# Optimization experiments

Hardware: AMD Instinct MI355X
Metric: run time of the kernel (lower is better)

The kernel has to match this reference:

```python
import jax, jax.numpy as jnp
import numpy as np
from jax import lax

D = 256
B, W = 16, 32


def setup_inputs() -> dict:
    key = jax.random.key(0)
    ks = jax.random.split(key, 5)
    x = jax.random.normal(ks[0], (B, D, W, W), dtype=jnp.float32)
    w_qkv = jax.random.normal(ks[1], (3 * D, D), dtype=jnp.float32) * (1.0 / np.sqrt(D))
    b_qkv = jax.random.normal(ks[2], (3 * D,), dtype=jnp.float32) * 0.01
    w_out = jax.random.normal(ks[3], (D, D, 3, 3), dtype=jnp.float32) * (1.0 / np.sqrt(9 * D))
    b_out = jax.random.normal(ks[4], (D,), dtype=jnp.float32) * 0.01
    alpha = jnp.ones((), dtype=jnp.float32)
    return {"x": x, "w_qkv": w_qkv, "b_qkv": b_qkv, "w_out": w_out, "b_out": b_out, "alpha": alpha}


def reference(x, w_qkv, b_qkv, w_out, b_out, alpha):
    Bb, C, H, Ww = x.shape  # C == D, H == Ww
    N = H * Ww
    # 1x1 conv qkv projection
    qkv = jnp.einsum('bchw,oc->bohw', x, w_qkv) + b_qkv[None, :, None, None]
    q, k, v = jnp.split(qkv, 3, axis=1)
    q = q.reshape(Bb, C, N)
    k = k.reshape(Bb, C, N)
    v = v.reshape(Bb, C, N)
    scale = 1.0 / (C ** 0.5)
    attn = jax.nn.softmax(jnp.einsum('bcq,bck->bqk', q, k) * scale, axis=-1)  # [B,N,N]
    # faithful to torch: (B,N,C) memory-reinterpreted to (B,C,H,W)
    out = jnp.einsum('bqk,bck->bqc', attn, v).reshape(Bb, C, H, Ww)
    x = x + alpha * jax.nn.relu(out)
    conv = lax.conv_general_dilated(
        x, w_out, window_strides=(1, 1), padding='SAME',
        dimension_numbers=('NCHW', 'OIHW', 'NCHW')) + b_out[None, :, None, None]
    x = x + alpha * jax.nn.relu(conv)
    return x
```

## Files before the change

kernel.cpp:

```cpp
#include <hip/hip_runtime.h>
#include <cmath>

namespace {

constexpr int Dc  = 256;
constexpr int NB  = 16;
constexpr int NSP = 1024;
constexpr int OC3 = 768;

typedef __attribute__((ext_vector_type(8))) short  short8;
typedef __attribute__((ext_vector_type(8))) ushort ushort8;
typedef __attribute__((ext_vector_type(4))) ushort ushort4_v;
typedef __attribute__((ext_vector_type(4))) float  f32x4;

__device__ inline ushort f2bf(float f) {
  unsigned u = __builtin_bit_cast(unsigned, f);
  unsigned r = (u + 0x7FFFu + ((u >> 16) & 1u)) >> 16;
  return (ushort)r;
}
__device__ inline float bf2f(ushort u) {
  return __builtin_bit_cast(float, (unsigned)u << 16);
}

__device__ __forceinline__ void dma16(const ushort* g, ushort* l) {
  __builtin_amdgcn_global_load_lds(
      (const __attribute__((address_space(1))) unsigned int*)(const void*)g,
      (__attribute__((address_space(3))) unsigned int*)(void*)l, 16, 0, 0);
}

template<int BM>
__device__ __forceinline__ void mfma_core(
    const ushort* __restrict__ Abase, int lda,
    const ushort* __restrict__ Bbase, int ldb,
    int m0, int n0, int K, f32x4 (&acc)[BM / 32][4])
{
  constexpr int MI    = BM / 32;
  constexpr int AI    = BM / 64;
  constexpr int NLOAD = AI + 2;
  constexpr int BUFSZ = BM * 32 + 128 * 32;
  __shared__ ushort LDS[3 * BUFSZ];

  const int t = threadIdx.x;
  const int lane = t & 63, wid = t >> 6;
  const int wm = (wid >> 1) * (BM / 2);
  const int wo = (wid & 1) * 64;
  const int lm = lane & 15, lk = lane >> 4;
  const int aph = lk ^ ((lm >> 1) & 3);

  const int lrow = lane >> 2;
  const int niter = K >> 5;

  auto issue = [&](int kk) {
    const int c0 = kk << 5;
    ushort* buf = &LDS[(kk % 3) * BUFSZ];
#pragma unroll
    for (int i = 0; i < AI; ++i) {
      const int r0 = (i * 4 + wid) * 16;
      const int row = r0 + lrow;
      const int chunk = (lane & 3) ^ ((row >> 1) & 3);
      dma16(Abase + (size_t)(m0 + row) * lda + c0 + chunk * 8, buf + r0 * 32);
    }
#pragma unroll
    for (int i = 0; i < 2; ++i) {
      const int r0 = (i * 4 + wid) * 16;
      const int row = r0 + lrow;
      const int chunk = (lane & 3) ^ ((row >> 1) & 3);
      dma16(Bbase + (size_t)(n0 + row) * ldb + c0 + chunk * 8,
            buf + BM * 32 + r0 * 32);
    }
  };

  issue(0);
  issue(1);

  for (int kk = 0; kk < niter; ++kk) {
    __builtin_amdgcn_sched_barrier(0);
    if (kk < niter - 1) {
      if constexpr (NLOAD == 4)
        asm volatile("s_waitcnt vmcnt(4) lgkmcnt(0)" ::: "memory");
      else
        asm volatile("s_waitcnt vmcnt(3) lgkmcnt(0)" ::: "memory");
    } else {
      asm volatile("s_waitcnt vmcnt(0) lgkmcnt(0)" ::: "memory");
    }
    __builtin_amdgcn_s_barrier();
    __builtin_amdgcn_sched_barrier(0);
    if (kk + 2 < niter) issue(kk + 2);

    const ushort* Ab = &LDS[(kk % 3) * BUFSZ];
    const ushort* Bb = Ab + BM * 32;
    short8 af[MI], bw[4];
#pragma unroll
    for (int mi = 0; mi < MI; ++mi)
      af[mi] = *(const short8*)&Ab[(wm + mi * 16 + lm) * 32 + aph * 8];
#pragma unroll
    for (int oi = 0; oi < 4; ++oi)
      bw[oi] = *(const short8*)&Bb[(wo + oi * 16 + lm) * 32 + aph * 8];
#pragma unroll
    for (int mi = 0; mi < MI; ++mi)
#pragma unroll
      for (int oi = 0; oi < 4; ++oi)
        acc[mi][oi] = __builtin_amdgcn_mfma_f32_16x16x32_bf16(
            af[mi], bw[oi], acc[mi][oi], 0, 0, 0);
  }
}

__global__ __launch_bounds__(256) void k0_prep(
    const float* __restrict__ x, const float* __restrict__ w_qkv,
    const float* __restrict__ w_out,
    ushort* __restrict__ xt, ushort* __restrict__ wb,
    ushort* __restrict__ w2b, float* __restrict__ rowsum,
    ushort* __restrict__ x1p)
{
  __shared__ ushort tr[64][72];
  int bid = blockIdx.x;
  const int t = threadIdx.x;
  if (bid < 768) {
    const int i = bid * 256 + t;
    wb[i] = f2bf(w_qkv[i]);
    if (i < NB * NSP) rowsum[i] = 0.0f;
    return;
  }
  bid -= 768;
  if (bid < 1024) {
    const int b  = bid >> 6;
    const int r  = bid & 63;
    const int c0 = (r >> 4) * 64;
    const int n0 = (r & 15) * 64;
    const float* xb = x + (size_t)b * Dc * NSP;
    const int nl4 = (t & 15) * 4, clb = t >> 4;
#pragma unroll
    for (int rr = 0; rr < 4; ++rr) {
      const int cl = clb + rr * 16;
      float4 xv = *(const float4*)(xb + (size_t)(c0 + cl) * NSP + n0 + nl4);
      tr[nl4 + 0][cl] = f2bf(xv.x);
      tr[nl4 + 1][cl] = f2bf(xv.y);
      tr[nl4 + 2][cl] = f2bf(xv.z);
      tr[nl4 + 3][cl] = f2bf(xv.w);
    }
    __syncthreads();
#pragma unroll
    for (int j = 0; j < 2; ++j) {
      const int s  = t + j * 256;
      const int nl = s >> 3, c8 = (s & 7) * 8;
      *(ushort8*)(xt + ((size_t)(b * NSP + n0 + nl)) * Dc + c0 + c8) =
          *(const ushort8*)&tr[nl][c8];
    }
    return;
  }
  bid -= 1024;
  if (bid < 256) {
    const int o  = bid;
    const int ic = t;
    const float* src = w_out + ((size_t)o * Dc + ic) * 9;
#pragma unroll
    for (int k9 = 0; k9 < 9; ++k9)
      w2b[((size_t)k9 * Dc + o) * Dc + ic] = f2bf(src[k9]);
    return;
  }
  bid -= 256;
  {
    ushort* p = x1p + (size_t)bid * 1156 * 256;
    for (int r = 0; r < 132; ++r) {
      int r34;
      if (r < 34)      r34 = r;
      else if (r < 68) r34 = 33 * 34 + (r - 34);
      else { const int rr = r - 68; r34 = (1 + (rr >> 1)) * 34 + (rr & 1) * 33; }
      p[(size_t)r34 * 256 + t] = 0;
    }
  }
}

__global__ __launch_bounds__(256) void k1a_qk(
    const ushort* __restrict__ wb, const ushort* __restrict__ xt,
    const float* __restrict__ b_qkv, ushort* __restrict__ qkt)
{
  const int b  = blockIdx.z;
  const int m0 = blockIdx.y * 128;
  const int n0 = blockIdx.x * 128;
  f32x4 acc[4][4];
#pragma unroll
  for (int i = 0; i < 4; ++i)
#pragma unroll
    for (int j = 0; j < 4; ++j) acc[i][j] = (f32x4)(0.0f);
  mfma_core<128>(wb, Dc, xt + (size_t)b * NSP * Dc, Dc, m0, n0, Dc, acc);
  const int t = threadIdx.x, lane = t & 63, wid = t >> 6;
  const int wm = (wid >> 1) * 64, wo = (wid & 1) * 64;
  const int lm = lane & 15, lk = lane >> 4;
  ushort* qb = qkt + (size_t)b * NSP * 512;
#pragma unroll
  for (int mi = 0; mi < 4; ++mi) {
    const int o = m0 + wm + mi * 16 + lk * 4;
    float4 bi = *(const float4*)(b_qkv + o);
#pragma unroll
    for (int oi = 0; oi < 4; ++oi) {
      const int n = n0 + wo + oi * 16 + lm;
      f32x4 a = acc[mi][oi];
      ushort4_v st = { f2bf(a.x + bi.x), f2bf(a.y + bi.y),
                       f2bf(a.z + bi.z), f2bf(a.w + bi.w) };
      *(ushort4_v*)(qb + (size_t)n * 512 + o) = st;
    }
  }
}

__global__ __launch_bounds__(256) void k1b_v(
    const ushort* __restrict__ wb, const ushort* __restrict__ xt,
    const float* __restrict__ b_qkv, ushort* __restrict__ vb)
{
  const int b  = blockIdx.z;
  const int m0 = blockIdx.y * 64;
  const int n0 = blockIdx.x * 128;
  f32x4 acc[2][4];
#pragma unroll
  for (int i = 0; i < 2; ++i)
#pragma unroll
    for (int j = 0; j < 4; ++j) acc[i][j] = (f32x4)(0.0f);
  mfma_core<64>(xt + (size_t)b * NSP * Dc, Dc, wb + 512 * Dc, Dc, m0, n0, Dc, acc);
  const int t = threadIdx.x, lane = t & 63, wid = t >> 6;
  const int wm = (wid >> 1) * 32, wo = (wid & 1) * 64;
  const int lm = lane & 15, lk = lane >> 4;
  ushort* vbb = vb + (size_t)b * Dc * NSP;
#pragma unroll
  for (int oi = 0; oi < 4; ++oi) {
    const int c = n0 + wo + oi * 16 + lm;
    const float bo = b_qkv[512 + c];
#pragma unroll
    for (int mi = 0; mi < 2; ++mi) {
      const int n = m0 + wm + mi * 16 + lk * 4;
      f32x4 a = acc[mi][oi];
      ushort4_v st = { f2bf(a.x + bo), f2bf(a.y + bo),
                       f2bf(a.z + bo), f2bf(a.w + bo) };
      *(ushort4_v*)(vbb + (size_t)c * NSP + n) = st;
    }
  }
}

__global__ __launch_bounds__(256) void k2m_exp(
    const ushort* __restrict__ qkt, ushort* __restrict__ E,
    float* __restrict__ rowsum)
{
  const int b  = blockIdx.z;
  const int m0 = blockIdx.y * 128;
  const int n0 = blockIdx.x * 128;
  const ushort* base = qkt + (size_t)b * NSP * 512;
  f32x4 acc[4][4];
#pragma unroll
  for (int i = 0; i < 4; ++i)
#pragma unroll
    for (int j = 0; j < 4; ++j) acc[i][j] = (f32x4)(0.0f);
  mfma_core<128>(base + 256, 512, base, 512, m0, n0, Dc, acc);
  const int t = threadIdx.x, lane = t & 63, wid = t >> 6;
  const int wm = (wid >> 1) * 64, wo = (wid & 1) * 64;
  const int lm = lane & 15, lk = lane >> 4;
  ushort* Eb = E + (size_t)b * NSP * NSP;
  float* rs = rowsum + (size_t)b * NSP;
#pragma unroll
  for (int oi = 0; oi < 4; ++oi) {
    const int q = n0 + wo + oi * 16 + lm;
    float ps = 0.0f;
#pragma unroll
    for (int mi = 0; mi < 4; ++mi) {
      const int kidx = m0 + wm + mi * 16 + lk * 4;
      f32x4 a = acc[mi][oi] * 0.0625f;
      float e0 = __expf(a.x), e1 = __expf(a.y);
      float e2 = __expf(a.z), e3 = __expf(a.w);
      ps += (e0 + e1) + (e2 + e3);
      ushort4_v st = { f2bf(e0), f2bf(e1), f2bf(e2), f2bf(e3) };
      *(ushort4_v*)(Eb + (size_t)q * NSP + kidx) = st;
    }
    ps += __shfl_xor(ps, 16);
    ps += __shfl_xor(ps, 32);
    if (lane < 16) atomicAdd(rs + q, ps);
  }
}

__global__ __launch_bounds__(256) void k4f_pv(
    const ushort* __restrict__ vb, const ushort* __restrict__ E,
    const float* __restrict__ rowsum, const ushort* __restrict__ xt,
    const float* __restrict__ alphap, ushort* __restrict__ x1p)
{
  const int b  = blockIdx.z;
  const int m0 = blockIdx.y * 64;
  const int n0 = blockIdx.x * 128;
  f32x4 acc[2][4];
#pragma unroll
  for (int i = 0; i < 2; ++i)
#pragma unroll
    for (int j = 0; j < 4; ++j) acc[i][j] = (f32x4)(0.0f);
  mfma_core<64>(vb + (size_t)b * Dc * NSP, NSP,
                E + (size_t)b * NSP * NSP, NSP, m0, n0, NSP, acc);

  __shared__ float T[64][133];
  const int t = threadIdx.x, lane = t & 63, wid = t >> 6;
  const int wm = (wid >> 1) * 32, wo = (wid & 1) * 64;
  const int lm = lane & 15, lk = lane >> 4;
  const float* rs = rowsum + (size_t)b * NSP;
#pragma unroll
  for (int oi = 0; oi < 4; ++oi) {
    const int ql = wo + oi * 16 + lm;
    const float inv = 1.0f / rs[n0 + ql];
#pragma unroll
    for (int mi = 0; mi < 2; ++mi) {
      const int cl = wm + mi * 16 + lk * 4;
      f32x4 a = acc[mi][oi] * inv;
      T[cl + 0][ql] = a.x;
      T[cl + 1][ql] = a.y;
      T[cl + 2][ql] = a.z;
      T[cl + 3][ql] = a.w;
    }
  }
  __syncthreads();

  const float al = *alphap;
  const int s = wid;
  const int c_off = lane;
  const int sp = s * 256 + m0 + c_off;
  const int r34 = ((sp >> 5) + 1) * 34 + (sp & 31) + 1;
  const int ch0 = n0 >> 2;
  const ushort* xtb = xt + (size_t)b * NSP * Dc + (size_t)sp * Dc + ch0;
  ushort* xpb = x1p + (size_t)b * 1156 * 256;
  ushort8 pack[4];
#pragma unroll
  for (int g = 0; g < 4; ++g) {
    ushort8 xv = *(const ushort8*)(xtb + g * 8);
#pragma unroll
    for (int e = 0; e < 8; ++e) {
      const int chl = g * 8 + e;
      const float v = T[c_off][4 * chl + s];
      pack[g][e] = f2bf(bf2f(xv[e]) + al * fmaxf(v, 0.f));
    }
  }
  ushort8* dst = (ushort8*)(xpb + (size_t)r34 * 256 + ch0);
#pragma unroll
  for (int g = 0; g < 4; ++g) dst[g] = pack[g];
}

__global__ __launch_bounds__(256) void k6_conv_mfma(
    const ushort* __restrict__ x1p, const ushort* __restrict__ w2b,
    const float* __restrict__ bout, const float* __restrict__ alphap,
    float* __restrict__ out)
{
  const int b  = blockIdx.z;
  const int n0 = blockIdx.x * 64;
  const int o0 = blockIdx.y * 128;
  __shared__ ushort LDS[3 * 12288];
  const int t = threadIdx.x;
  const int lane = t & 63, wid = t >> 6;
  const int wm = (wid >> 1) * 32, wo = (wid & 1) * 64;
  const int lm = lane & 15, lk = lane >> 4;
  const int aphr = lm & 7;

  const int lrow   = wid * 8 + (lane >> 3);
  const int lchunk = ((lane & 7) ^ (lane >> 3)) * 8;

  const ushort* xp = x1p + (size_t)b * 1156 * 256;
  const int nA0 = n0 + lrow;
  const int r34A0 = ((nA0 >> 5) + 1) * 34 + (nA0 & 31) + 1;
  const ushort* Ag0 = xp + (size_t)r34A0 * 256 + lchunk;
  const ushort* Ag1 = Ag0 + (size_t)34 * 256;
  const ushort* Wg  = w2b + (size_t)(o0 + lrow) * 256 + lchunk;

  auto issue = [&](int kt) {
    const int buf = kt % 3;
    const int k9 = kt >> 2;
    const int dh = ((k9 * 11) >> 5) - 1;
    const int dw = k9 - (dh + 1) * 3 - 1;
    const int aoff = (dh * 34 + dw) * 256 + ((kt & 3) << 6);
    const size_t woff = (size_t)k9 * 65536 + ((kt & 3) << 6);
    ushort* lb = &LDS[buf * 12288 + wid * 512];
    dma16(Ag0 + aoff, lb);
    dma16(Ag1 + aoff, lb + 2048);
#pragma unroll
    for (int i = 0; i < 4; ++i)
      dma16(Wg + woff + i * 8192, lb + 4096 + i * 2048);
  };

  f32x4 acc[2][4];
#pragma unroll
  for (int i = 0; i < 2; ++i)
#pragma unroll
    for (int j = 0; j < 4; ++j) acc[i][j] = (f32x4)(0.0f);

  issue(0);
  issue(1);

  for (int kt = 0; kt < 36; ++kt) {
    __builtin_amdgcn_sched_barrier(0);
    if (kt < 35)
      asm volatile("s_waitcnt vmcnt(6) lgkmcnt(0)" ::: "memory");
    else
      asm volatile("s_waitcnt vmcnt(0) lgkmcnt(0)" ::: "memory");
    __builtin_amdgcn_s_barrier();
    __builtin_amdgcn_sched_barrier(0);
    if (kt + 2 < 36) issue(kt + 2);

    const ushort* Ab = &LDS[(kt % 3) * 12288];
    const ushort* Wb = Ab + 4096;
#pragma unroll
    for (int s = 0; s < 2; ++s) {
      const int ph = ((s << 2) | lk) ^ aphr;
      short8 af[2], bw[4];
#pragma unroll
      for (int mi = 0; mi < 2; ++mi)
        af[mi] = *(const short8*)&Ab[(wm + mi * 16 + lm) * 64 + ph * 8];
#pragma unroll
      for (int oi = 0; oi < 4; ++oi)
        bw[oi] = *(const short8*)&Wb[(wo + oi * 16 + lm) * 64 + ph * 8];
#pragma unroll
      for (int mi = 0; mi < 2; ++mi)
#pragma unroll
        for (int oi = 0; oi < 4; ++oi)
          acc[mi][oi] = __builtin_amdgcn_mfma_f32_16x16x32_bf16(
              af[mi], bw[oi], acc[mi][oi], 0, 0, 0);
    }
  }

  const float al = *alphap;
  float* ob = out + (size_t)b * Dc * NSP;
#pragma unroll
  for (int oi = 0; oi < 4; ++oi) {
    const int o = o0 + wo + oi * 16 + lm;
    const float bo = bout[o];
#pragma unroll
    for (int mi = 0; mi < 2; ++mi) {
      const int nr = n0 + wm + mi * 16 + lk * 4;
      const int r34 = ((nr >> 5) + 1) * 34 + (nr & 31) + 1;
      const ushort* xr = xp + (size_t)r34 * 256 + o;
      f32x4 a = acc[mi][oi];
      float4 r;
      r.x = bf2f(xr[0])   + al * fmaxf(a.x + bo, 0.f);
      r.y = bf2f(xr[256]) + al * fmaxf(a.y + bo, 0.f);
      r.z = bf2f(xr[512]) + al * fmaxf(a.z + bo, 0.f);
      r.w = bf2f(xr[768]) + al * fmaxf(a.w + bo, 0.f);
      *(float4*)(ob + (size_t)o * NSP + nr) = r;
    }
  }
}

}

extern "C" void kernel_launch(void* const* d_in, const int* in_sizes, int n_in,
                              void* d_out, int out_size, void* d_ws, size_t ws_size,
                              hipStream_t stream)
{
  const float* x     = (const float*)d_in[0];
  const float* w_qkv = (const float*)d_in[1];
  const float* b_qkv = (const float*)d_in[2];
  const float* w_out = (const float*)d_in[3];
  const float* b_out = (const float*)d_in[4];
  const float* alpha = (const float*)d_in[5];
  float* out = (float*)d_out;

  char* ws = (char*)d_ws;
  ushort* qkt  = (ushort*)ws;
  ushort* vb   = (ushort*)(ws + (16u << 20));
  ushort* xt   = (ushort*)(ws + (24u << 20));
  ushort* wb   = (ushort*)(ws + (32u << 20));
  float*  rowsum = (float*)(ws + (32u << 20) + (1u << 19));
  ushort* E    = (ushort*)(ws + (33u << 20));
  ushort* w2b  = (ushort*)(ws + (65u << 20));
  ushort* x1p  = (ushort*)(ws + (67u << 20));

  k0_prep     <<<dim3(2064),       256, 0, stream>>>(x, w_qkv, w_out,
                                                     xt, wb, w2b, rowsum, x1p);
  k1a_qk      <<<dim3(8, 4, 16),   256, 0, stream>>>(wb, xt, b_qkv, qkt);
  k1b_v       <<<dim3(2, 16, 16),  256, 0, stream>>>(wb, xt, b_qkv, vb);
  k2m_exp     <<<dim3(8, 8, 16),   256, 0, stream>>>(qkt, E, rowsum);
  k4f_pv      <<<dim3(8, 4, 16),   256, 0, stream>>>(vb, E, rowsum, xt, alpha, x1p);
  k6_conv_mfma<<<dim3(16, 2, 16),  256, 0, stream>>>(x1p, w2b, b_out, alpha, out);
}
```

Baseline: 102.4 us.

## Merge QK and V projection kernels; enlarge conv tile to 128x128 with K=32 steps

The Q/K and V projection GEMMs are merged into one launch, with the V part now using 128x128 tiles, so one dispatch covers all projection work. The 3x3 conv kernel moves from 64x128 output tiles with 64-wide K slices to 128x128 tiles with 32-wide K slices. It uses a new LDS swizzle and 72 pipeline steps, giving more MFMA work per loaded byte. The tradeoff is fewer conv blocks (256), more accumulator registers per thread, and twice as many barrier-synchronised K iterations.

```diff
diff --git a/kernel.cpp b/kernel.cpp
--- a/kernel.cpp
+++ b/kernel.cpp
@@ -171,66 +171,60 @@
   }
 }
 
-__global__ __launch_bounds__(256) void k1a_qk(
+__global__ __launch_bounds__(256) void k1ab(
     const ushort* __restrict__ wb, const ushort* __restrict__ xt,
-    const float* __restrict__ b_qkv, ushort* __restrict__ qkt)
-{
-  const int b  = blockIdx.z;
-  const int m0 = blockIdx.y * 128;
-  const int n0 = blockIdx.x * 128;
-  f32x4 acc[4][4];
-#pragma unroll
-  for (int i = 0; i < 4; ++i)
-#pragma unroll
-    for (int j = 0; j < 4; ++j) acc[i][j] = (f32x4)(0.0f);
-  mfma_core<128>(wb, Dc, xt + (size_t)b * NSP * Dc, Dc, m0, n0, Dc, acc);
+    const float* __restrict__ b_qkv, ushort* __restrict__ qkt,
+    ushort* __restrict__ vb)
+{
+  const int bid = blockIdx.x;
   const int t = threadIdx.x, lane = t & 63, wid = t >> 6;
   const int wm = (wid >> 1) * 64, wo = (wid & 1) * 64;
   const int lm = lane & 15, lk = lane >> 4;
-  ushort* qb = qkt + (size_t)b * NSP * 512;
-#pragma unroll
-  for (int mi = 0; mi < 4; ++mi) {
-    const int o = m0 + wm + mi * 16 + lk * 4;
-    float4 bi = *(const float4*)(b_qkv + o);
+  f32x4 acc[4][4];
+#pragma unroll
+  for (int i = 0; i < 4; ++i)
+#pragma unroll
+    for (int j = 0; j < 4; ++j) acc[i][j] = (f32x4)(0.0f);
+
+  if (bid < 512) {
+    const int b = bid >> 5, r = bid & 31;
+    const int m0 = (r >> 3) * 128;
+    const int n0 = (r & 7) * 128;
+    mfma_core<128>(wb, Dc, xt + (size_t)b * NSP * Dc, Dc, m0, n0, Dc, acc);
+    ushort* qb = qkt + (size_t)b * NSP * 512;
+#pragma unroll
+    for (int mi = 0; mi < 4; ++mi) {
+      const int o = m0 + wm + mi * 16 + lk * 4;
+      float4 bi = *(const float4*)(b_qkv + o);
+#pragma unroll
+      for (int oi = 0; oi < 4; ++oi) {
+        const int n = n0 + wo + oi * 16 + lm;
+        f32x4 a = acc[mi][oi];
+        ushort4_v st = { f2bf(a.x + bi.x), f2bf(a.y + bi.y),
+                         f2bf(a.z + bi.z), f2bf(a.w + bi.w) };
+        *(ushort4_v*)(qb + (size_t)n * 512 + o) = st;
+      }
+    }
+  } else {
+    const int q = bid - 512;
+    const int b = q >> 4, r = q & 15;
+    const int m0 = (r >> 1) * 128;
+    const int n0 = (r & 1) * 128;
+    mfma_core<128>(xt + (size_t)b * NSP * Dc, Dc, wb + 512 * Dc, Dc,
+                   m0, n0, Dc, acc);
+    ushort* vbb = vb + (size_t)b * Dc * NSP;
 #pragma unroll
     for (int oi = 0; oi < 4; ++oi) {
-      const int n = n0 + wo + oi * 16 + lm;
-      f32x4 a = acc[mi][oi];
-      ushort4_v st = { f2bf(a.x + bi.x), f2bf(a.y + bi.y),
-                       f2bf(a.z + bi.z), f2bf(a.w + bi.w) };
-      *(ushort4_v*)(qb + (size_t)n * 512 + o) = st;
-    }
-  }
-}
-
-__global__ __launch_bounds__(256) void k1b_v(
-    const ushort* __restrict__ wb, const ushort* __restrict__ xt,
-    const float* __restrict__ b_qkv, ushort* __restrict__ vb)
-{
-  const int b  = blockIdx.z;
-  const int m0 = blockIdx.y * 64;
-  const int n0 = blockIdx.x * 128;
-  f32x4 acc[2][4];
-#pragma unroll
-  for (int i = 0; i < 2; ++i)
-#pragma unroll
-    for (int j = 0; j < 4; ++j) acc[i][j] = (f32x4)(0.0f);
-  mfma_core<64>(xt + (size_t)b * NSP * Dc, Dc, wb + 512 * Dc, Dc, m0, n0, Dc, acc);
-  const int t = threadIdx.x, lane = t & 63, wid = t >> 6;
-  const int wm = (wid >> 1) * 32, wo = (wid & 1) * 64;
-  const int lm = lane & 15, lk = lane >> 4;
-  ushort* vbb = vb + (size_t)b * Dc * NSP;
-#pragma unroll
-  for (int oi = 0; oi < 4; ++oi) {
-    const int c = n0 + wo + oi * 16 + lm;
-    const float bo = b_qkv[512 + c];
-#pragma unroll
-    for (int mi = 0; mi < 2; ++mi) {
-      const int n = m0 + wm + mi * 16 + lk * 4;
-      f32x4 a = acc[mi][oi];
-      ushort4_v st = { f2bf(a.x + bo), f2bf(a.y + bo),
-                       f2bf(a.z + bo), f2bf(a.w + bo) };
-      *(ushort4_v*)(vbb + (size_t)c * NSP + n) = st;
+      const int c = n0 + wo + oi * 16 + lm;
+      const float bo = b_qkv[512 + c];
+#pragma unroll
+      for (int mi = 0; mi < 4; ++mi) {
+        const int n = m0 + wm + mi * 16 + lk * 4;
+        f32x4 a = acc[mi][oi];
+        ushort4_v st = { f2bf(a.x + bo), f2bf(a.y + bo),
+                         f2bf(a.z + bo), f2bf(a.w + bo) };
+        *(ushort4_v*)(vbb + (size_t)c * NSP + n) = st;
+      }
     }
   }
 }
@@ -341,78 +335,76 @@
     float* __restrict__ out)
 {
   const int b  = blockIdx.z;
-  const int n0 = blockIdx.x * 64;
+  const int n0 = blockIdx.x * 128;
   const int o0 = blockIdx.y * 128;
-  __shared__ ushort LDS[3 * 12288];
+  __shared__ ushort LDS[3 * 8192];
   const int t = threadIdx.x;
   const int lane = t & 63, wid = t >> 6;
-  const int wm = (wid >> 1) * 32, wo = (wid & 1) * 64;
+  const int wm = (wid >> 1) * 64, wo = (wid & 1) * 64;
   const int lm = lane & 15, lk = lane >> 4;
-  const int aphr = lm & 7;
-
-  const int lrow   = wid * 8 + (lane >> 3);
-  const int lchunk = ((lane & 7) ^ (lane >> 3)) * 8;
+  const int aph = lk ^ ((lm >> 1) & 3);
 
   const ushort* xp = x1p + (size_t)b * 1156 * 256;
-  const int nA0 = n0 + lrow;
-  const int r34A0 = ((nA0 >> 5) + 1) * 34 + (nA0 & 31) + 1;
-  const ushort* Ag0 = xp + (size_t)r34A0 * 256 + lchunk;
-  const ushort* Ag1 = Ag0 + (size_t)34 * 256;
-  const ushort* Wg  = w2b + (size_t)(o0 + lrow) * 256 + lchunk;
+  const int row0 = wid * 32 + (lane >> 2);
+  const int row1 = row0 + 16;
+  const int ck0 = ((lane & 3) ^ ((row0 >> 1) & 3)) * 8;
+  const int ck1 = ((lane & 3) ^ ((row1 >> 1) & 3)) * 8;
+  const int nA0 = n0 + row0, nA1 = n0 + row1;
+  const ushort* Ag0 = xp + (size_t)(((nA0 >> 5) + 1) * 34 + (nA0 & 31) + 1) * 256 + ck0;
+  const ushort* Ag1 = xp + (size_t)(((nA1 >> 5) + 1) * 34 + (nA1 & 31) + 1) * 256 + ck1;
+  const ushort* Wg0 = w2b + (size_t)(o0 + row0) * 256 + ck0;
+  const ushort* Wg1 = w2b + (size_t)(o0 + row1) * 256 + ck1;
 
   auto issue = [&](int kt) {
-    const int buf = kt % 3;
-    const int k9 = kt >> 2;
+    ushort* buf = &LDS[(kt % 3) * 8192];
+    const int k9 = kt >> 3;
     const int dh = ((k9 * 11) >> 5) - 1;
     const int dw = k9 - (dh + 1) * 3 - 1;
-    const int aoff = (dh * 34 + dw) * 256 + ((kt & 3) << 6);
-    const size_t woff = (size_t)k9 * 65536 + ((kt & 3) << 6);
-    ushort* lb = &LDS[buf * 12288 + wid * 512];
-    dma16(Ag0 + aoff, lb);
-    dma16(Ag1 + aoff, lb + 2048);
-#pragma unroll
-    for (int i = 0; i < 4; ++i)
-      dma16(Wg + woff + i * 8192, lb + 4096 + i * 2048);
+    const int c0 = (kt & 7) << 5;
+    const int aoff = (dh * 34 + dw) * 256 + c0;
+    const size_t woff = (size_t)k9 * 65536 + c0;
+    ushort* ab = buf + (wid * 32) * 32;
+    dma16(Ag0 + aoff, ab);
+    dma16(Ag1 + aoff, ab + 512);
+    ushort* wbuf = buf + 4096 + (wid * 32) * 32;
+    dma16(Wg0 + woff, wbuf);
+    dma16(Wg1 + woff, wbuf + 512);
   };
 
-  f32x4 acc[2][4];
-#pragma unroll
-  for (int i = 0; i < 2; ++i)
+  f32x4 acc[4][4];
+#pragma unroll
+  for (int i = 0; i < 4; ++i)
 #pragma unroll
     for (int j = 0; j < 4; ++j) acc[i][j] = (f32x4)(0.0f);
 
   issue(0);
   issue(1);
 
-  for (int kt = 0; kt < 36; ++kt) {
+  for (int kt = 0; kt < 72; ++kt) {
     __builtin_amdgcn_sched_barrier(0);
-    if (kt < 35)
-      asm volatile("s_waitcnt vmcnt(6) lgkmcnt(0)" ::: "memory");
+    if (kt < 71)
+      asm volatile("s_waitcnt vmcnt(4) lgkmcnt(0)" ::: "memory");
     else
       asm volatile("s_waitcnt vmcnt(0) lgkmcnt(0)" ::: "memory");
     __builtin_amdgcn_s_barrier();
     __builtin_amdgcn_sched_barrier(0);
-    if (kt + 2 < 36) issue(kt + 2);
-
-    const ushort* Ab = &LDS[(kt % 3) * 12288];
+    if (kt + 2 < 72) issue(kt + 2);
+
+    const ushort* Ab = &LDS[(kt % 3) * 8192];
     const ushort* Wb = Ab + 4096;
-#pragma unroll
-    for (int s = 0; s < 2; ++s) {
-      const int ph = ((s << 2) | lk) ^ aphr;
-      short8 af[2], bw[4];
-#pragma unroll
-      for (int mi = 0; mi < 2; ++mi)
-        af[mi] = *(const short8*)&Ab[(wm + mi * 16 + lm) * 64 + ph * 8];
+    short8 af[4], bw[4];
+#pragma unroll
+    for (int mi = 0; mi < 4; ++mi)
+      af[mi] = *(const short8*)&Ab[(wm + mi * 16 + lm) * 32 + aph * 8];
+#pragma unroll
+    for (int oi = 0; oi < 4; ++oi)
+      bw[oi] = *(const short8*)&Wb[(wo + oi * 16 + lm) * 32 + aph * 8];
+#pragma unroll
+    for (int mi = 0; mi < 4; ++mi)
 #pragma unroll
       for (int oi = 0; oi < 4; ++oi)
-        bw[oi] = *(const short8*)&Wb[(wo + oi * 16 + lm) * 64 + ph * 8];
-#pragma unroll
-      for (int mi = 0; mi < 2; ++mi)
-#pragma unroll
-        for (int oi = 0; oi < 4; ++oi)
-          acc[mi][oi] = __builtin_amdgcn_mfma_f32_16x16x32_bf16(
-              af[mi], bw[oi], acc[mi][oi], 0, 0, 0);
-    }
+        acc[mi][oi] = __builtin_amdgcn_mfma_f32_16x16x32_bf16(
+            af[mi], bw[oi], acc[mi][oi], 0, 0, 0);
   }
 
   const float al = *alphap;
@@ -422,7 +414,7 @@
     const int o = o0 + wo + oi * 16 + lm;
     const float bo = bout[o];
 #pragma unroll
-    for (int mi = 0; mi < 2; ++mi) {
+    for (int mi = 0; mi < 4; ++mi) {
       const int nr = n0 + wm + mi * 16 + lk * 4;
       const int r34 = ((nr >> 5) + 1) * 34 + (nr & 31) + 1;
       const ushort* xr = xp + (size_t)r34 * 256 + o;
@@ -463,9 +455,8 @@
 
   k0_prep     <<<dim3(2064),       256, 0, stream>>>(x, w_qkv, w_out,
                                                      xt, wb, w2b, rowsum, x1p);
-  k1a_qk      <<<dim3(8, 4, 16),   256, 0, stream>>>(wb, xt, b_qkv, qkt);
-  k1b_v       <<<dim3(2, 16, 16),  256, 0, stream>>>(wb, xt, b_qkv, vb);
+  k1ab        <<<dim3(768),        256, 0, stream>>>(wb, xt, b_qkv, qkt, vb);
   k2m_exp     <<<dim3(8, 8, 16),   256, 0, stream>>>(qkt, E, rowsum);
   k4f_pv      <<<dim3(8, 4, 16),   256, 0, stream>>>(vb, E, rowsum, xt, alpha, x1p);
-  k6_conv_mfma<<<dim3(16, 2, 16),  256, 0, stream>>>(x1p, w2b, b_out, alpha, out);
-}
+  k6_conv_mfma<<<dim3(8, 2, 16),   256, 0, stream>>>(x1p, w2b, b_out, alpha, out);
+}
```

Result: slower. 105.1 us (+2.6%).
